# Kernel tuning notes

Measured on AMD Instinct MI355X. Metric: run time of the kernel, lower is better.

The kernel has to match this reference:

```python
import jax, jax.numpy as jnp
import numpy as np

LAMDA = 0.05
BETA = 1.0
FULL = 256          # full image / k-space size
SAMP = 128          # sampled k-space size
OFF_R, OFF_C = 3, 3 # sampling offsets from cop.Sample(3, 3, ...)
IR = (OFF_R + 2 * jnp.arange(SAMP)) % FULL  # row sample indices (stride 2)
IC = (OFF_C + 2 * jnp.arange(SAMP)) % FULL  # col sample indices


def dwt2(x):
    # single-level orthonormal 2D Haar DWT, quadrant layout [LL LH; HL HH]
    a = x[..., ::2, ::2]; b = x[..., ::2, 1::2]
    c = x[..., 1::2, ::2]; d = x[..., 1::2, 1::2]
    ll = (a + b + c + d) * 0.5
    lh = (a - b + c - d) * 0.5
    hl = (a + b - c - d) * 0.5
    hh = (a - b - c + d) * 0.5
    top = jnp.concatenate([ll, lh], axis=-1)
    bot = jnp.concatenate([hl, hh], axis=-1)
    return jnp.concatenate([top, bot], axis=-2)


def idwt2(w):
    H = w.shape[-2] // 2; W = w.shape[-1] // 2
    ll = w[..., :H, :W]; lh = w[..., :H, W:]
    hl = w[..., H:, :W]; hh = w[..., H:, W:]
    a = (ll + lh + hl + hh) * 0.5
    b = (ll - lh + hl - hh) * 0.5
    c = (ll + lh - hl - hh) * 0.5
    d = (ll - lh - hl + hh) * 0.5
    x = jnp.zeros(w.shape, w.dtype)
    x = x.at[..., ::2, ::2].set(a)
    x = x.at[..., ::2, 1::2].set(b)
    x = x.at[..., 1::2, ::2].set(c)
    x = x.at[..., 1::2, 1::2].set(d)
    return x


def shrink(x, t):
    # soft-thresholding (prox of t*|x|_1)
    return jnp.sign(x) * jnp.maximum(jnp.abs(x) - t, 0.0)


def sample(x):
    # gather strided k-space samples: [..., 256, 256] -> [..., 128, 128]
    return x[..., IR[:, None], IC[None, :]]


def sample_t(v):
    # adjoint: scatter samples back into zero-filled full grid
    full = jnp.zeros(v.shape[:-2] + (FULL, FULL), v.dtype)
    return full.at[..., IR[:, None], IC[None, :]].set(v)


def setup_inputs() -> dict:
    key = jax.random.key(0)
    k1, k2 = jax.random.split(key)
    s = jax.random.normal(k1, (256, SAMP, SAMP), dtype=jnp.float32)
    image = jax.random.normal(k2, (256, FULL, FULL), dtype=jnp.float32)
    return {"s": s, "image": image}


def reference(s, image):
    thresh = 1.0 / BETA
    coeff = LAMDA / BETA
    dwt_x = dwt2(image)
    new_alpha = shrink(dwt_x, thresh)
    # new_v = dwt_x - new_alpha; idwt(new_alpha - new_v) = idwt(2*alpha - dwt_x)
    idwtx = idwt2(2.0 * new_alpha - dwt_x)
    y = jnp.fft.fft2(idwtx) + coeff * sample_t(s)
    y = y + coeff * sample_t(sample(y))
    return jnp.fft.ifft2(y)
```

## Files before the change

### kernel.cpp

```cpp
#include <hip/hip_runtime.h>


__device__ __forceinline__ float fwv(float w) {
    float sh = fmaxf(fabsf(w) - 1.0f, 0.0f);
    return 2.0f * copysignf(sh, w) - w;
}

__device__ __forceinline__ int bitrev7(int x) {
    return (int)(__builtin_bitreverse32((unsigned)x) >> 25);
}

__global__ __launch_bounds__(1024) void fused_kernel(const float* __restrict__ s,
                                                     const float* __restrict__ image,
                                                     float* __restrict__ outf,
                                                     int out_floats)
{
    __shared__ float2 A[128 * 128];

    const int tid  = threadIdx.x;
    const int lane = tid & 63;
    const int wave = tid >> 6;
    const int b    = blockIdx.x;
    const float PI_F   = 3.14159265358979323846f;
    const float TWO_PI = 6.2831853071795864769f;

    float twc[7], tws[7];
    #pragma unroll
    for (int k = 0; k < 7; ++k) {
        int h = 64 >> k;
        float th = PI_F * (float)(lane & (h - 1)) / (float)h;
        __sincosf(th, &tws[k], &twc[k]);
    }

#define FFT128()                                                                     \
    do {                                                                             \
        { float ar = x0r, ai = x0i, br = x1r, bi = x1i;                              \
          x0r = ar + br; x0i = ai + bi;                                              \
          float dr = ar - br, di = ai - bi;                                          \
          x1r = dr * twc[0] - di * tws[0];                                           \
          x1i = dr * tws[0] + di * twc[0]; }                                         \
        _Pragma("unroll")                                                            \
        for (int k = 1; k < 7; ++k) {                                                \
            int h = 64 >> k;                                                         \
            bool hi = (lane & h) != 0;                                               \
            float wc = twc[k], ws = tws[k];                                          \
            { float rr = __shfl_xor(x0r, h), ri = __shfl_xor(x0i, h);                \
              float sr = hi ? (rr - x0r) : (x0r + rr);                               \
              float si = hi ? (ri - x0i) : (x0i + ri);                               \
              float tr = sr * wc - si * ws, ti = sr * ws + si * wc;                  \
              x0r = hi ? tr : sr; x0i = hi ? ti : si; }                              \
            { float rr = __shfl_xor(x1r, h), ri = __shfl_xor(x1i, h);                \
              float sr = hi ? (rr - x1r) : (x1r + rr);                               \
              float si = hi ? (ri - x1i) : (x1i + ri);                               \
              float tr = sr * wc - si * ws, ti = sr * ws + si * wc;                  \
              x1r = hi ? tr : sr; x1i = hi ? ti : si; }                              \
        }                                                                            \
    } while (0)

    const float* sb = s + (size_t)b * (128 * 128);
    const int p0 = lane, p1 = 64 | lane;

    const int m6   = (int)(__builtin_bitreverse32((unsigned)lane) >> 26);
    const int prt0 = (int)(__builtin_bitreverse32((unsigned)((64 - m6) & 63)) >> 26);

    #pragma unroll 2
    for (int t = 0; t < 4; ++t) {
        int ia = (wave << 3) | (t << 1);
        int ib = ia | 1;
        float x0r = sb[ia * 128 + lane];
        float x0i = sb[ib * 128 + lane];
        float x1r = sb[ia * 128 + 64 + lane];
        float x1i = sb[ib * 128 + 64 + lane];
        FFT128();
        float c0r = __shfl(x0r, prt0), c0i = __shfl(x0i, prt0);
        float a0r = 0.5f * (x0r + c0r), a0i = 0.5f * (x0i - c0i);
        float b0r = 0.5f * (x0i + c0i), b0i = 0.5f * (c0r - x0r);
        float c1r = __shfl_xor(x1r, 63), c1i = __shfl_xor(x1i, 63);
        float a1r = 0.5f * (x1r + c1r), a1i = 0.5f * (x1i - c1i);
        float b1r = 0.5f * (x1i + c1i), b1i = 0.5f * (c1r - x1r);
        A[p0 * 128 + ((ia ^ p0) & 127)] = make_float2(a0r, a0i);
        A[p0 * 128 + ((ib ^ p0) & 127)] = make_float2(b0r, b0i);
        A[p1 * 128 + ((ia ^ p1) & 127)] = make_float2(a1r, a1i);
        A[p1 * 128 + ((ib ^ p1) & 127)] = make_float2(b1r, b1i);
    }
    __syncthreads();

    #pragma unroll 2
    for (int t = 0; t < 8; ++t) {
        int vp = (wave << 3) | t;
        float2 a0 = A[vp * 128 + ((p0 ^ vp) & 127)];
        float2 a1 = A[vp * 128 + ((p1 ^ vp) & 127)];
        float x0r = a0.x, x0i = a0.y, x1r = a1.x, x1i = a1.y;
        FFT128();
        A[vp * 128 + ((p0 ^ vp) & 127)] = make_float2(x0r, x0i);
        A[vp * 128 + ((p1 ^ vp) & 127)] = make_float2(x1r, x1i);
    }
    __syncthreads();

    const float  c0    = 0.0125f;
    const float  kappa = 0.0525f / 65536.0f;
    const size_t obase = (size_t)b * 65536;
    const float2* ib2 = (const float2*)(image + (size_t)b * 65536);

    for (int qd = tid; qd < 4096; qd += 1024) {
        int p = qd >> 6;
        int q = qd & 63;

        float D[2][2][2][2];
        #pragma unroll
        for (int Aq = 0; Aq < 2; ++Aq) {
            #pragma unroll
            for (int Bq = 0; Bq < 2; ++Bq) {
                int P = p + 64 * Aq, Q = q + 64 * Bq;
                float2 t0 = ib2[(2 * P) * 128 + Q];
                float2 t1 = ib2[(2 * P + 1) * 128 + Q];
                float a = t0.x, bb = t0.y, cc = t1.x, dd = t1.y;
                float wll = (a + bb + cc + dd) * 0.5f;
                float wlh = (a - bb + cc - dd) * 0.5f;
                float whl = (a + bb - cc - dd) * 0.5f;
                float whh = (a - bb - cc + dd) * 0.5f;
                float vll = fwv(wll), vlh = fwv(wlh), vhl = fwv(whl), vhh = fwv(whh);
                D[Aq][Bq][0][0] = (vll + vlh + vhl + vhh) * 0.5f;
                D[Aq][Bq][0][1] = (vll - vlh + vhl - vhh) * 0.5f;
                D[Aq][Bq][1][0] = (vll + vlh - vhl - vhh) * 0.5f;
                D[Aq][Bq][1][1] = (vll - vlh - vhl + vhh) * 0.5f;
            }
        }
        float S[2][2];
        #pragma unroll
        for (int r = 0; r < 2; ++r)
            #pragma unroll
            for (int c = 0; c < 2; ++c)
                S[r][c] = D[0][0][r][c] - D[1][0][r][c] - D[0][1][r][c] + D[1][1][r][c];

        int ru0 = bitrev7(2 * p), ru1 = bitrev7(2 * p + 1);
        int rv0 = bitrev7(2 * q), rv1 = bitrev7(2 * q + 1);
        float2 Tv[2][2];
        Tv[0][0] = A[rv0 * 128 + ((ru0 ^ rv0) & 127)];
        Tv[0][1] = A[rv1 * 128 + ((ru0 ^ rv1) & 127)];
        Tv[1][0] = A[rv0 * 128 + ((ru1 ^ rv0) & 127)];
        Tv[1][1] = A[rv1 * 128 + ((ru1 ^ rv1) & 127)];

        float2 phv[3];
        #pragma unroll
        for (int k = 0; k < 3; ++k) {
            float ps, pc;
            __sincosf((TWO_PI * 3.0f / 256.0f) * (float)(2 * p + 2 * q + k), &ps, &pc);
            phv[k] = make_float2(pc, ps);
        }

        #pragma unroll
        for (int Aq = 0; Aq < 2; ++Aq) {
            #pragma unroll
            for (int Bq = 0; Bq < 2; ++Bq) {
                float kq = ((Aq + Bq) & 1) ? -kappa : kappa;
                float sS = ((Aq ^ Bq) & 1) ? -c0 : c0;
                int nrow = 2 * p + 128 * Aq;
                int mcol = 2 * q + 128 * Bq;
                #pragma unroll
                for (int r = 0; r < 2; ++r) {
                    float2 ph0 = phv[r];
                    float2 ph1 = phv[r + 1];
                    float2 wv;
                    wv.x = D[Aq][Bq][r][0] + sS * S[r][0]
                         + kq * (ph0.x * Tv[r][0].x - ph0.y * Tv[r][0].y);
                    wv.y = D[Aq][Bq][r][1] + sS * S[r][1]
                         + kq * (ph1.x * Tv[r][1].x - ph1.y * Tv[r][1].y);
                    size_t fi = obase + (size_t)((nrow + r) * 256 + mcol);
                    if (fi + 2 <= (size_t)out_floats)
                        *(float2*)&outf[fi] = wv;
                }
            }
        }
    }
#undef FFT128
}

extern "C" void kernel_launch(void* const* d_in, const int* in_sizes, int n_in,
                              void* d_out, int out_size, void* d_ws, size_t ws_size,
                              hipStream_t stream)
{
    const float* s     = (const float*)d_in[0];
    const float* image = (const float*)d_in[1];
    float*       outf  = (float*)d_out;
    hipLaunchKernelGGL(fused_kernel, dim3(256), dim3(1024), 0, stream,
                       s, image, outf, out_size);
}
```

Measured before the change: 139.2 us.

## Prefetch image tile into registers before FFT and tabulate phase twiddles in LDS

Hoists all per-thread image loads to the start of the kernel so the global-memory latency overlaps the two FFT passes, instead of loading after the FFT barrier. Replaces per-element sincos phase computation with a 256-entry shared-memory table and hoists the column bit-reversal out of the loop. Also drops the output bounds check and adds a launch-bounds occupancy hint. Holding 32 float2 per thread in registers across the FFT raises register pressure and may cause spills with 1024-thread blocks.

```diff
diff --git a/kernel.cpp b/kernel.cpp
--- a/kernel.cpp
+++ b/kernel.cpp
@@ -10,12 +10,12 @@
     return (int)(__builtin_bitreverse32((unsigned)x) >> 25);
 }
 
-__global__ __launch_bounds__(1024) void fused_kernel(const float* __restrict__ s,
-                                                     const float* __restrict__ image,
-                                                     float* __restrict__ outf,
-                                                     int out_floats)
+__global__ __launch_bounds__(1024, 4) void fused_kernel(const float* __restrict__ s,
+                                                        const float* __restrict__ image,
+                                                        float* __restrict__ outf)
 {
     __shared__ float2 A[128 * 128];
+    __shared__ float2 ph_tab[256];
 
     const int tid  = threadIdx.x;
     const int lane = tid & 63;
@@ -23,6 +23,29 @@
     const int b    = blockIdx.x;
     const float PI_F   = 3.14159265358979323846f;
     const float TWO_PI = 6.2831853071795864769f;
+
+    const float2* ib2 = (const float2*)(image + (size_t)b * 65536);
+    const int q  = tid & 63;
+    const int pw = tid >> 6;
+    float2 img[4][8];
+    #pragma unroll
+    for (int it = 0; it < 4; ++it) {
+        int p = (it << 4) | pw;
+        #pragma unroll
+        for (int Aq = 0; Aq < 2; ++Aq)
+            #pragma unroll
+            for (int Bq = 0; Bq < 2; ++Bq)
+                #pragma unroll
+                for (int r = 0; r < 2; ++r)
+                    img[it][(Aq << 2) | (Bq << 1) | r] =
+                        ib2[(2 * (p + 64 * Aq) + r) * 128 + (q + 64 * Bq)];
+    }
+
+    if (tid < 256) {
+        float ps, pc;
+        __sincosf((TWO_PI * 3.0f / 256.0f) * (float)tid, &ps, &pc);
+        ph_tab[tid] = make_float2(pc, ps);
+    }
 
     float twc[7], tws[7];
     #pragma unroll
@@ -66,11 +89,11 @@
     #pragma unroll 2
     for (int t = 0; t < 4; ++t) {
         int ia = (wave << 3) | (t << 1);
-        int ib = ia | 1;
+        int ic = ia | 1;
         float x0r = sb[ia * 128 + lane];
-        float x0i = sb[ib * 128 + lane];
+        float x0i = sb[ic * 128 + lane];
         float x1r = sb[ia * 128 + 64 + lane];
-        float x1i = sb[ib * 128 + 64 + lane];
+        float x1i = sb[ic * 128 + 64 + lane];
         FFT128();
         float c0r = __shfl(x0r, prt0), c0i = __shfl(x0i, prt0);
         float a0r = 0.5f * (x0r + c0r), a0i = 0.5f * (x0i - c0i);
@@ -79,9 +102,9 @@
         float a1r = 0.5f * (x1r + c1r), a1i = 0.5f * (x1i - c1i);
         float b1r = 0.5f * (x1i + c1i), b1i = 0.5f * (c1r - x1r);
         A[p0 * 128 + ((ia ^ p0) & 127)] = make_float2(a0r, a0i);
-        A[p0 * 128 + ((ib ^ p0) & 127)] = make_float2(b0r, b0i);
+        A[p0 * 128 + ((ic ^ p0) & 127)] = make_float2(b0r, b0i);
         A[p1 * 128 + ((ia ^ p1) & 127)] = make_float2(a1r, a1i);
-        A[p1 * 128 + ((ib ^ p1) & 127)] = make_float2(b1r, b1i);
+        A[p1 * 128 + ((ic ^ p1) & 127)] = make_float2(b1r, b1i);
     }
     __syncthreads();
 
@@ -100,20 +123,19 @@
     const float  c0    = 0.0125f;
     const float  kappa = 0.0525f / 65536.0f;
     const size_t obase = (size_t)b * 65536;
-    const float2* ib2 = (const float2*)(image + (size_t)b * 65536);
-
-    for (int qd = tid; qd < 4096; qd += 1024) {
-        int p = qd >> 6;
-        int q = qd & 63;
+    const int rv0 = bitrev7(2 * q), rv1 = bitrev7(2 * q + 1);
+
+    #pragma unroll
+    for (int it = 0; it < 4; ++it) {
+        int p = (it << 4) | pw;
 
         float D[2][2][2][2];
         #pragma unroll
         for (int Aq = 0; Aq < 2; ++Aq) {
             #pragma unroll
             for (int Bq = 0; Bq < 2; ++Bq) {
-                int P = p + 64 * Aq, Q = q + 64 * Bq;
-                float2 t0 = ib2[(2 * P) * 128 + Q];
-                float2 t1 = ib2[(2 * P + 1) * 128 + Q];
+                float2 t0 = img[it][(Aq << 2) | (Bq << 1)];
+                float2 t1 = img[it][(Aq << 2) | (Bq << 1) | 1];
                 float a = t0.x, bb = t0.y, cc = t1.x, dd = t1.y;
                 float wll = (a + bb + cc + dd) * 0.5f;
                 float wlh = (a - bb + cc - dd) * 0.5f;
@@ -134,20 +156,14 @@
                 S[r][c] = D[0][0][r][c] - D[1][0][r][c] - D[0][1][r][c] + D[1][1][r][c];
 
         int ru0 = bitrev7(2 * p), ru1 = bitrev7(2 * p + 1);
-        int rv0 = bitrev7(2 * q), rv1 = bitrev7(2 * q + 1);
         float2 Tv[2][2];
         Tv[0][0] = A[rv0 * 128 + ((ru0 ^ rv0) & 127)];
         Tv[0][1] = A[rv1 * 128 + ((ru0 ^ rv1) & 127)];
         Tv[1][0] = A[rv0 * 128 + ((ru1 ^ rv0) & 127)];
         Tv[1][1] = A[rv1 * 128 + ((ru1 ^ rv1) & 127)];
 
-        float2 phv[3];
-        #pragma unroll
-        for (int k = 0; k < 3; ++k) {
-            float ps, pc;
-            __sincosf((TWO_PI * 3.0f / 256.0f) * (float)(2 * p + 2 * q + k), &ps, &pc);
-            phv[k] = make_float2(pc, ps);
-        }
+        int tbase = 2 * p + 2 * q;
+        float2 phv[3] = { ph_tab[tbase], ph_tab[tbase + 1], ph_tab[tbase + 2] };
 
         #pragma unroll
         for (int Aq = 0; Aq < 2; ++Aq) {
@@ -166,9 +182,7 @@
                          + kq * (ph0.x * Tv[r][0].x - ph0.y * Tv[r][0].y);
                     wv.y = D[Aq][Bq][r][1] + sS * S[r][1]
                          + kq * (ph1.x * Tv[r][1].x - ph1.y * Tv[r][1].y);
-                    size_t fi = obase + (size_t)((nrow + r) * 256 + mcol);
-                    if (fi + 2 <= (size_t)out_floats)
-                        *(float2*)&outf[fi] = wv;
+                    *(float2*)&outf[obase + (size_t)((nrow + r) * 256 + mcol)] = wv;
                 }
             }
         }
@@ -184,5 +198,5 @@
     const float* image = (const float*)d_in[1];
     float*       outf  = (float*)d_out;
     hipLaunchKernelGGL(fused_kernel, dim3(256), dim3(1024), 0, stream,
-                       s, image, outf, out_size);
-}
+                       s, image, outf);
+}
```

New measurement: 138.8 us. About the same (-0.3%).
